# Kernel tuning notes

Hardware: AMD Instinct MI355X
Metric: run time of the kernel (lower is better)

The kernel has to match this reference:

```python
import jax, jax.numpy as jnp
import numpy as np

B, S, D = 4, 4096, 1024
BLOCK_LEN = 128
NUM_BLOCKS = S // BLOCK_LEN  # 32


def setup_inputs() -> dict:
    key = jax.random.key(0)
    k0, k1, k2 = jax.random.split(key, 3)
    x = jax.random.normal(k0, (B, S, D), dtype=jnp.float32)
    # nn.Linear weights stored as (in, out) for x @ W + b convention
    Wqkv = jax.random.normal(k1, (D, 3 * D), dtype=jnp.float32) * (1.0 / np.sqrt(D))
    bqkv = jnp.zeros((3 * D,), dtype=jnp.float32)
    Wout = jax.random.normal(k2, (D, D), dtype=jnp.float32) * (1.0 / np.sqrt(D))
    bout = jnp.zeros((D,), dtype=jnp.float32)
    return {"x": x, "Wqkv": Wqkv, "bqkv": bqkv, "Wout": Wout, "bout": bout}


def _causal_attn(q, k, v):
    # q,k,v: (..., L, D); single-head SDPA with scale 1/sqrt(D), causal mask
    d = q.shape[-1]
    L = q.shape[-2]
    scale = 1.0 / np.sqrt(d)
    scores = jnp.einsum('...qd,...kd->...qk', q, k) * jnp.asarray(scale, q.dtype)
    mask = jnp.tril(jnp.ones((L, L), dtype=bool))
    neg = jnp.asarray(jnp.finfo(scores.dtype).min, scores.dtype)
    scores = jnp.where(mask, scores, neg)
    p = jax.nn.softmax(scores, axis=-1)
    return jnp.einsum('...qk,...kd->...qd', p, v)


def reference(x, Wqkv, bqkv, Wout, bout):
    b, s, d = x.shape
    nb = s // BLOCK_LEN
    x2 = x.reshape(b, nb, BLOCK_LEN, d)              # (B, NB, BL, D)
    qkv = x2 @ Wqkv + bqkv                            # (B, NB, BL, 3D)
    q, k, v = jnp.split(qkv, 3, axis=-1)
    # 'column' attention: attend across blocks at the same within-block position
    q = q.transpose(0, 2, 1, 3)                       # (B, BL, NB, D)
    k = k.transpose(0, 2, 1, 3)
    v = v.transpose(0, 2, 1, 3)
    out = _causal_attn(q, k, v)                       # (B, BL, NB, D)
    out = out.transpose(0, 2, 1, 3).reshape(b, s, d)  # back to (B, S, D)
    return out @ Wout + bout
```

## Files before the change

kernel.cpp:

```cpp
#include <hip/hip_runtime.h>
#include <math.h>

#define BB   4
#define SS   4096
#define DD   1024
#define BL   128
#define NB   32

typedef __attribute__((ext_vector_type(4))) float f32x4;
typedef __attribute__((ext_vector_type(16))) float f32x16;
typedef __attribute__((ext_vector_type(8))) short bf16x8;
typedef __attribute__((ext_vector_type(8))) unsigned short u16x8;

__device__ __forceinline__ float bf2f(unsigned short u) {
    return __uint_as_float(((unsigned int)u) << 16);
}
__device__ __forceinline__ unsigned short f2bf(float f) {
    unsigned int u = __float_as_uint(f);
    return (unsigned short)((u + 0x7FFFu + ((u >> 16) & 1u)) >> 16);
}
__device__ __forceinline__ void gload_lds16(const unsigned short* g, unsigned short* l) {
    __builtin_amdgcn_global_load_lds(
        (const __attribute__((address_space(1))) void*)g,
        (__attribute__((address_space(3))) void*)l, 16, 0, 0);
}

__global__ __launch_bounds__(256) void cvt_f32_bf16(const float4* __restrict__ in,
                                                    ushort4* __restrict__ out, int n4) {
    int i = blockIdx.x * 256 + threadIdx.x;
    if (i < n4) {
        float4 v = in[i];
        ushort4 o;
        o.x = f2bf(v.x); o.y = f2bf(v.y); o.z = f2bf(v.z); o.w = f2bf(v.w);
        out[i] = o;
    }
}

__global__ __launch_bounds__(256) void transcvt(const float* __restrict__ W,
                                                unsigned short* __restrict__ WT,
                                                int K, int N) {
    __shared__ float tile[32][33];
    const int n0 = blockIdx.x * 32, k0 = blockIdx.y * 32;
    const int tx = threadIdx.x & 31, ty = threadIdx.x >> 5;
    #pragma unroll
    for (int r = 0; r < 32; r += 8)
        tile[ty + r][tx] = W[(size_t)(k0 + ty + r) * N + n0 + tx];
    __syncthreads();
    #pragma unroll
    for (int r = 0; r < 32; r += 8)
        WT[(size_t)(n0 + ty + r) * K + k0 + tx] = f2bf(tile[tx][ty + r]);
}

#define GBAR() __builtin_amdgcn_s_barrier()
#define LGKM0() do { asm volatile("s_waitcnt lgkmcnt(0)" ::: "memory"); \
                     __builtin_amdgcn_sched_barrier(0); } while (0)

#define MFMA_PAIR(q, ni) \
    acc[(q)*2+0][ni] = __builtin_amdgcn_mfma_f32_16x16x32_bf16(a[0][0], breg[ni][0], acc[(q)*2+0][ni], 0, 0, 0); \
    acc[(q)*2+0][ni] = __builtin_amdgcn_mfma_f32_16x16x32_bf16(a[0][1], breg[ni][1], acc[(q)*2+0][ni], 0, 0, 0); \
    acc[(q)*2+1][ni] = __builtin_amdgcn_mfma_f32_16x16x32_bf16(a[1][0], breg[ni][0], acc[(q)*2+1][ni], 0, 0, 0); \
    acc[(q)*2+1][ni] = __builtin_amdgcn_mfma_f32_16x16x32_bf16(a[1][1], breg[ni][1], acc[(q)*2+1][ni], 0, 0, 0);

#define MFMA_Q(q) do { \
    __builtin_amdgcn_s_setprio(1); \
    MFMA_PAIR(q, 0) MFMA_PAIR(q, 1) MFMA_PAIR(q, 2) MFMA_PAIR(q, 3) \
    __builtin_amdgcn_s_setprio(0); } while (0)

#define LOAD_A(q) do { \
    a[0][0] = *(const bf16x8*)(pA + ((q)*2+0)*1024 + sw0); \
    a[0][1] = *(const bf16x8*)(pA + ((q)*2+0)*1024 + sw1); \
    a[1][0] = *(const bf16x8*)(pA + ((q)*2+1)*1024 + sw0); \
    a[1][1] = *(const bf16x8*)(pA + ((q)*2+1)*1024 + sw1); } while (0)

template<typename OutT>
__global__ __launch_bounds__(512, 2) void gemm256(
    const unsigned short* __restrict__ A, const unsigned short* __restrict__ BT,
    const float* __restrict__ bias, OutT* __restrict__ C,
    int M, int N, int K, int ntn)
{
    __shared__ __align__(16) unsigned short smem[65536];
    unsigned short* sAb = smem;
    unsigned short* sBb = smem + 32768;

    const int nwg = gridDim.x;
    const int wg  = blockIdx.x;
    const int swzb = (wg & 7) * (nwg >> 3) + (wg >> 3);
    const int m0 = (swzb / ntn) * 256, n0 = (swzb % ntn) * 256;

    const int t    = threadIdx.x;
    const int w    = t >> 6;
    const int lane = t & 63;
    const int wm   = w >> 2, wn = w & 3;

    const int srow8 = lane >> 3;
    const int sgch  = (lane & 7) ^ srow8;
    const int NT    = K >> 6;

    auto STAGE_A = [&](int ts, int cb) {
        const int r = cb + (w << 3);
        gload_lds16(A + (size_t)(m0 + r + srow8) * K + (ts << 6) + sgch * 8,
                    sAb + (size_t)(ts & 1) * 16384 + r * 64);
    };
    auto STAGE_B = [&](int ts, int cb) {
        const int r = cb + (w << 3);
        gload_lds16(BT + (size_t)(n0 + r + srow8) * K + (ts << 6) + sgch * 8,
                    sBb + (size_t)(ts & 1) * 16384 + r * 64);
    };

    const int frA = wm * 128 + (lane & 15);
    const int frB = wn * 64  + (lane & 15);
    const int sw0 = (((lane >> 4) + 0) ^ (lane & 7)) * 8;
    const int sw1 = (((lane >> 4) + 4) ^ (lane & 7)) * 8;

    f32x4 acc[8][4];
    #pragma unroll
    for (int i = 0; i < 8; ++i)
        #pragma unroll
        for (int j = 0; j < 4; ++j) acc[i][j] = (f32x4){0.f, 0.f, 0.f, 0.f};

    STAGE_B(0, 0); STAGE_B(0, 64); STAGE_B(0, 128); STAGE_B(0, 192);
    STAGE_A(0, 0); STAGE_A(0, 64); STAGE_A(0, 128); STAGE_A(0, 192);
    asm volatile("s_waitcnt vmcnt(4)" ::: "memory");
    if (NT > 1) {
        STAGE_B(1, 0); STAGE_B(1, 64); STAGE_B(1, 128); STAGE_B(1, 192);
        STAGE_A(1, 0); STAGE_A(1, 128);
        asm volatile("s_waitcnt vmcnt(6)" ::: "memory");
    } else {
        asm volatile("s_waitcnt vmcnt(0)" ::: "memory");
    }
    GBAR();

    for (int ts = 0; ts < NT; ++ts) {
        const unsigned short* pA = sAb + (size_t)(ts & 1) * 16384 + frA * 64;
        const unsigned short* pB = sBb + (size_t)(ts & 1) * 16384 + frB * 64;
        bf16x8 breg[4][2];
        bf16x8 a[2][2];

        #pragma unroll
        for (int ni = 0; ni < 4; ++ni) {
            breg[ni][0] = *(const bf16x8*)(pB + ni * 1024 + sw0);
            breg[ni][1] = *(const bf16x8*)(pB + ni * 1024 + sw1);
        }
        LOAD_A(0);
        if (ts + 1 < NT) { STAGE_A(ts + 1, 64); STAGE_A(ts + 1, 192); }
        GBAR(); LGKM0(); MFMA_Q(0); GBAR();

        LOAD_A(1);
        if (ts + 2 < NT) { STAGE_B(ts + 2, 0); STAGE_B(ts + 2, 64); }
        GBAR(); LGKM0(); MFMA_Q(1); GBAR();

        LOAD_A(2);
        if (ts + 2 < NT) { STAGE_B(ts + 2, 128); STAGE_B(ts + 2, 192); }
        GBAR(); LGKM0(); MFMA_Q(2); GBAR();

        LOAD_A(3);
        if (ts + 2 < NT) { STAGE_A(ts + 2, 0); STAGE_A(ts + 2, 128); }
        GBAR(); LGKM0(); MFMA_Q(3);
        if (ts + 2 < NT) asm volatile("s_waitcnt vmcnt(6)" ::: "memory");
        else             asm volatile("s_waitcnt vmcnt(0)" ::: "memory");
        GBAR();
    }

    if constexpr (sizeof(OutT) == 2) {
        unsigned short (*cb)[256] = (unsigned short (*)[256])smem;
        #pragma unroll
        for (int ni = 0; ni < 4; ++ni) {
            const int col = wn * 64 + ni * 16 + (lane & 15);
            const float bv = bias[n0 + col];
            #pragma unroll
            for (int mi = 0; mi < 8; ++mi) {
                const int rb = wm * 128 + mi * 16 + ((lane >> 4) << 2);
                #pragma unroll
                for (int r = 0; r < 4; ++r)
                    cb[rb + r][col] = f2bf(acc[mi][ni][r] + bv);
            }
        }
        __syncthreads();
        unsigned short* Cp = (unsigned short*)C;
        #pragma unroll
        for (int it = 0; it < 16; ++it) {
            const int row = it * 16 + (t >> 5);
            const int cs  = (t & 31) * 8;
            u16x8 v = *(const u16x8*)&cb[row][cs];
            *(u16x8*)(Cp + (size_t)(m0 + row) * N + n0 + cs) = v;
        }
    } else {
        float (*cf)[256] = (float (*)[256])smem;
        #pragma unroll
        for (int h = 0; h < 2; ++h) {
            if (wm == h) {
                #pragma unroll
                for (int ni = 0; ni < 4; ++ni) {
                    const int col = wn * 64 + ni * 16 + (lane & 15);
                    const float bv = bias[n0 + col];
                    #pragma unroll
                    for (int mi = 0; mi < 8; ++mi) {
                        const int rb = mi * 16 + ((lane >> 4) << 2);
                        #pragma unroll
                        for (int r = 0; r < 4; ++r)
                            cf[rb + r][col] = acc[mi][ni][r] + bv;
                    }
                }
            }
            __syncthreads();
            float* Cp = (float*)C;
            #pragma unroll
            for (int it = 0; it < 16; ++it) {
                const int row = it * 8 + (t >> 6);
                const int c4  = (t & 63) * 4;
                float4 v = *(const float4*)&cf[row][c4];
                *(float4*)(Cp + (size_t)(m0 + h * 128 + row) * N + n0 + c4) = v;
            }
            __syncthreads();
        }
    }
}

__global__ __launch_bounds__(256) void col_attn_mfma(const unsigned short* __restrict__ qkv,
                                                     unsigned short* __restrict__ outb)
{
    const int b  = blockIdx.x >> 7;
    const int bl = blockIdx.x & (BL - 1);

    __shared__ float red[4][32][33];
    __shared__ float p_s[NB][NB + 1];

    const int t    = threadIdx.x;
    const int w    = t >> 6;
    const int lane = t & 63;

    const size_t rowstride = (size_t)BL * 3 * DD;
    const unsigned short* base = qkv + ((size_t)b * NB * BL + bl) * (3 * DD);

    {
        const int arow = lane & 31;
        const int khi  = (lane >> 5) * 8;
        const unsigned short* qp = base + (size_t)arow * rowstride + w * 256 + khi;
        const unsigned short* kp = qp + DD;

        f32x16 acc0 = {}, acc1 = {};
        #pragma unroll
        for (int s = 0; s < 16; s += 2) {
            bf16x8 aq0 = *(const bf16x8*)(qp + s * 16);
            bf16x8 bk0 = *(const bf16x8*)(kp + s * 16);
            bf16x8 aq1 = *(const bf16x8*)(qp + s * 16 + 16);
            bf16x8 bk1 = *(const bf16x8*)(kp + s * 16 + 16);
            acc0 = __builtin_amdgcn_mfma_f32_32x32x16_bf16(aq0, bk0, acc0, 0, 0, 0);
            acc1 = __builtin_amdgcn_mfma_f32_32x32x16_bf16(aq1, bk1, acc1, 0, 0, 0);
        }
        const int ccol = lane & 31;
        const int rhi  = (lane >> 5) * 4;
        #pragma unroll
        for (int r = 0; r < 16; ++r) {
            const int crow = (r & 3) + 8 * (r >> 2) + rhi;
            red[w][crow][ccol] = acc0[r] + acc1[r];
        }
    }
    __syncthreads();

    {
        const float scale = 1.0f / 32.0f;
        const int row = t >> 3;
        const int c0  = (t & 7) * 4;
        #pragma unroll
        for (int j = 0; j < 4; ++j) {
            const int c = c0 + j;
            p_s[row][c] = (red[0][row][c] + red[1][row][c] +
                           red[2][row][c] + red[3][row][c]) * scale;
        }
    }
    __syncthreads();

    if (t < NB) {
        const int i = t;
        float mx = p_s[i][0];
        for (int j = 1; j <= i; ++j) mx = fmaxf(mx, p_s[i][j]);
        float sum = 0.f;
        for (int j = 0; j <= i; ++j) { float e = __expf(p_s[i][j] - mx); p_s[i][j] = e; sum += e; }
        const float inv = 1.0f / sum;
        for (int j = 0; j <= i; ++j) p_s[i][j] *= inv;
        for (int j = i + 1; j < NB; ++j) p_s[i][j] = 0.f;
    }
    __syncthreads();

    const int d0v = t * 4;
    const unsigned short* vbase = base + 2 * DD;
    #pragma unroll 1
    for (int p = 0; p < 4; ++p) {
        float4 acc[8];
        #pragma unroll
        for (int ii = 0; ii < 8; ++ii) acc[ii] = make_float4(0.f, 0.f, 0.f, 0.f);
        const int jmax = (p + 1) * 8;
        for (int j = 0; j < jmax; ++j) {
            ushort4 v4 = *(const ushort4*)(vbase + (size_t)j * rowstride + d0v);
            const float vx = bf2f(v4.x), vy = bf2f(v4.y), vz = bf2f(v4.z), vw = bf2f(v4.w);
            #pragma unroll
            for (int ii = 0; ii < 8; ++ii) {
                const float pij = p_s[p * 8 + ii][j];
                acc[ii].x += pij * vx;
                acc[ii].y += pij * vy;
                acc[ii].z += pij * vz;
                acc[ii].w += pij * vw;
            }
        }
        #pragma unroll
        for (int ii = 0; ii < 8; ++ii) {
            const int i = p * 8 + ii;
            ushort4 o;
            o.x = f2bf(acc[ii].x); o.y = f2bf(acc[ii].y);
            o.z = f2bf(acc[ii].z); o.w = f2bf(acc[ii].w);
            *(ushort4*)(outb + ((size_t)(b * NB + i) * BL + bl) * DD + d0v) = o;
        }
    }
}

extern "C" void kernel_launch(void* const* d_in, const int* in_sizes, int n_in,
                              void* d_out, int out_size, void* d_ws, size_t ws_size,
                              hipStream_t stream) {
    (void)in_sizes; (void)n_in; (void)out_size; (void)ws_size;
    const float* x    = (const float*)d_in[0];
    const float* Wqkv = (const float*)d_in[1];
    const float* bqkv = (const float*)d_in[2];
    const float* Wout = (const float*)d_in[3];
    const float* bout = (const float*)d_in[4];
    float* out = (float*)d_out;

    char* ws = (char*)d_ws;
    unsigned short* xb    = (unsigned short*)ws;
    unsigned short* WqkvT = (unsigned short*)(ws + ((size_t)32 << 20));
    unsigned short* WoutT = (unsigned short*)(ws + ((size_t)38 << 20));
    unsigned short* qkvb  = (unsigned short*)(ws + ((size_t)40 << 20));
    unsigned short* attnb = (unsigned short*)(ws + ((size_t)136 << 20));

    const int M = BB * SS;

    cvt_f32_bf16<<<dim3((M * DD / 4 + 255) / 256), dim3(256), 0, stream>>>(
        (const float4*)x, (ushort4*)xb, M * DD / 4);
    transcvt<<<dim3(3 * DD / 32, DD / 32), dim3(256), 0, stream>>>(Wqkv, WqkvT, DD, 3 * DD);
    transcvt<<<dim3(DD / 32, DD / 32), dim3(256), 0, stream>>>(Wout, WoutT, DD, DD);

    gemm256<unsigned short><<<dim3((M / 256) * (3 * DD / 256)), dim3(512), 0, stream>>>(
        xb, WqkvT, bqkv, qkvb, M, 3 * DD, DD, 3 * DD / 256);

    col_attn_mfma<<<dim3(BB * BL), dim3(256), 0, stream>>>(qkvb, attnb);

    gemm256<float><<<dim3((M / 256) * (DD / 256)), dim3(512), 0, stream>>>(
        attnb, WoutT, bout, out, M, DD, DD, DD / 256);
}
```

Baseline: 216.5 us.

## Fuse fp32-to-bf16 conversion of x into the QKV GEMM A-tile staging

Drops the separate cvt_f32_bf16 kernel. The QKV GEMM now reads fp32 x directly through registers, converts to bf16 and writes the swizzled tile into LDS, interleaved across the four MFMA quarter-steps. This removes one kernel launch and the write and re-read of a 32MB bf16 copy of x. In exchange the A loads become register-staged rather than direct global-to-LDS, which raises register pressure and can expose load latency, since the explicit vmcnt waits are dropped for this path.

```diff
diff --git a/kernel.cpp b/kernel.cpp
--- a/kernel.cpp
+++ b/kernel.cpp
@@ -23,17 +23,6 @@
     __builtin_amdgcn_global_load_lds(
         (const __attribute__((address_space(1))) void*)g,
         (__attribute__((address_space(3))) void*)l, 16, 0, 0);
-}
-
-__global__ __launch_bounds__(256) void cvt_f32_bf16(const float4* __restrict__ in,
-                                                    ushort4* __restrict__ out, int n4) {
-    int i = blockIdx.x * 256 + threadIdx.x;
-    if (i < n4) {
-        float4 v = in[i];
-        ushort4 o;
-        o.x = f2bf(v.x); o.y = f2bf(v.y); o.z = f2bf(v.z); o.w = f2bf(v.w);
-        out[i] = o;
-    }
 }
 
 __global__ __launch_bounds__(256) void transcvt(const float* __restrict__ W,
@@ -51,6 +40,7 @@
         WT[(size_t)(n0 + ty + r) * K + k0 + tx] = f2bf(tile[tx][ty + r]);
 }
 
+
 #define GBAR() __builtin_amdgcn_s_barrier()
 #define LGKM0() do { asm volatile("s_waitcnt lgkmcnt(0)" ::: "memory"); \
                      __builtin_amdgcn_sched_barrier(0); } while (0)
@@ -72,9 +62,10 @@
     a[1][0] = *(const bf16x8*)(pA + ((q)*2+1)*1024 + sw0); \
     a[1][1] = *(const bf16x8*)(pA + ((q)*2+1)*1024 + sw1); } while (0)
 
-template<typename OutT>
+template<typename OutT, bool AF32>
 __global__ __launch_bounds__(512, 2) void gemm256(
-    const unsigned short* __restrict__ A, const unsigned short* __restrict__ BT,
+    const unsigned short* __restrict__ Abf, const float* __restrict__ Af,
+    const unsigned short* __restrict__ BT,
     const float* __restrict__ bias, OutT* __restrict__ C,
     int M, int N, int K, int ntn)
 {
@@ -98,7 +89,7 @@
 
     auto STAGE_A = [&](int ts, int cb) {
         const int r = cb + (w << 3);
-        gload_lds16(A + (size_t)(m0 + r + srow8) * K + (ts << 6) + sgch * 8,
+        gload_lds16(Abf + (size_t)(m0 + r + srow8) * K + (ts << 6) + sgch * 8,
                     sAb + (size_t)(ts & 1) * 16384 + r * 64);
     };
     auto STAGE_B = [&](int ts, int cb) {
@@ -106,6 +97,19 @@
         gload_lds16(BT + (size_t)(n0 + r + srow8) * K + (ts << 6) + sgch * 8,
                     sBb + (size_t)(ts & 1) * 16384 + r * 64);
     };
+    auto ISSUE_AQ = [&](int q, int ts1, float4& ra, float4& rb) {
+        const float* g = Af + (size_t)(m0 + q * 64 + (w << 3) + srow8) * K
+                         + (ts1 << 6) + sgch * 8;
+        ra = *(const float4*)g;
+        rb = *(const float4*)(g + 4);
+    };
+    auto WRITE_AQ = [&](int q, int ts1, const float4& ra, const float4& rb) {
+        u16x8 o;
+        o[0] = f2bf(ra.x); o[1] = f2bf(ra.y); o[2] = f2bf(ra.z); o[3] = f2bf(ra.w);
+        o[4] = f2bf(rb.x); o[5] = f2bf(rb.y); o[6] = f2bf(rb.z); o[7] = f2bf(rb.w);
+        *(u16x8*)(sAb + (size_t)(ts1 & 1) * 16384
+                  + (q * 64 + (w << 3) + srow8) * 64 + (lane & 7) * 8) = o;
+    };
 
     const int frA = wm * 128 + (lane & 15);
     const int frB = wn * 64  + (lane & 15);
@@ -118,15 +122,28 @@
         #pragma unroll
         for (int j = 0; j < 4; ++j) acc[i][j] = (f32x4){0.f, 0.f, 0.f, 0.f};
 
-    STAGE_B(0, 0); STAGE_B(0, 64); STAGE_B(0, 128); STAGE_B(0, 192);
-    STAGE_A(0, 0); STAGE_A(0, 64); STAGE_A(0, 128); STAGE_A(0, 192);
-    asm volatile("s_waitcnt vmcnt(4)" ::: "memory");
-    if (NT > 1) {
-        STAGE_B(1, 0); STAGE_B(1, 64); STAGE_B(1, 128); STAGE_B(1, 192);
-        STAGE_A(1, 0); STAGE_A(1, 128);
-        asm volatile("s_waitcnt vmcnt(6)" ::: "memory");
+    float4 r0a, r0b, r1a, r1b;
+
+    if constexpr (AF32) {
+        STAGE_B(0, 0); STAGE_B(0, 64); STAGE_B(0, 128); STAGE_B(0, 192);
+        if (NT > 1) { STAGE_B(1, 0); STAGE_B(1, 64); STAGE_B(1, 128); STAGE_B(1, 192); }
+        float4 p0a, p0b, p1a, p1b, p2a, p2b, p3a, p3b;
+        ISSUE_AQ(0, 0, p0a, p0b); ISSUE_AQ(1, 0, p1a, p1b);
+        ISSUE_AQ(2, 0, p2a, p2b); ISSUE_AQ(3, 0, p3a, p3b);
+        WRITE_AQ(0, 0, p0a, p0b); WRITE_AQ(1, 0, p1a, p1b);
+        WRITE_AQ(2, 0, p2a, p2b); WRITE_AQ(3, 0, p3a, p3b);
+        LGKM0();
     } else {
-        asm volatile("s_waitcnt vmcnt(0)" ::: "memory");
+        STAGE_B(0, 0); STAGE_B(0, 64); STAGE_B(0, 128); STAGE_B(0, 192);
+        STAGE_A(0, 0); STAGE_A(0, 64); STAGE_A(0, 128); STAGE_A(0, 192);
+        asm volatile("s_waitcnt vmcnt(4)" ::: "memory");
+        if (NT > 1) {
+            STAGE_B(1, 0); STAGE_B(1, 64); STAGE_B(1, 128); STAGE_B(1, 192);
+            STAGE_A(1, 0); STAGE_A(1, 128);
+            asm volatile("s_waitcnt vmcnt(6)" ::: "memory");
+        } else {
+            asm volatile("s_waitcnt vmcnt(0)" ::: "memory");
+        }
     }
     GBAR();
 
@@ -142,22 +159,37 @@
             breg[ni][1] = *(const bf16x8*)(pB + ni * 1024 + sw1);
         }
         LOAD_A(0);
-        if (ts + 1 < NT) { STAGE_A(ts + 1, 64); STAGE_A(ts + 1, 192); }
+        if constexpr (AF32) {
+            if (ts + 1 < NT) ISSUE_AQ(0, ts + 1, r0a, r0b);
+            if (ts > 0)      WRITE_AQ(3, ts, r1a, r1b);
+        } else {
+            if (ts + 1 < NT) { STAGE_A(ts + 1, 64); STAGE_A(ts + 1, 192); }
+        }
         GBAR(); LGKM0(); MFMA_Q(0); GBAR();
 
         LOAD_A(1);
+        if constexpr (AF32) { if (ts + 1 < NT) ISSUE_AQ(1, ts + 1, r1a, r1b); }
         if (ts + 2 < NT) { STAGE_B(ts + 2, 0); STAGE_B(ts + 2, 64); }
+        if constexpr (AF32) { if (ts + 1 < NT) WRITE_AQ(0, ts + 1, r0a, r0b); }
         GBAR(); LGKM0(); MFMA_Q(1); GBAR();
 
         LOAD_A(2);
+        if constexpr (AF32) { if (ts + 1 < NT) ISSUE_AQ(2, ts + 1, r0a, r0b); }
         if (ts + 2 < NT) { STAGE_B(ts + 2, 128); STAGE_B(ts + 2, 192); }
+        if constexpr (AF32) { if (ts + 1 < NT) WRITE_AQ(1, ts + 1, r1a, r1b); }
         GBAR(); LGKM0(); MFMA_Q(2); GBAR();
 
         LOAD_A(3);
-        if (ts + 2 < NT) { STAGE_A(ts + 2, 0); STAGE_A(ts + 2, 128); }
+        if constexpr (AF32) {
+            if (ts + 1 < NT) { ISSUE_AQ(3, ts + 1, r1a, r1b); WRITE_AQ(2, ts + 1, r0a, r0b); }
+        } else {
+            if (ts + 2 < NT) { STAGE_A(ts + 2, 0); STAGE_A(ts + 2, 128); }
+        }
         GBAR(); LGKM0(); MFMA_Q(3);
-        if (ts + 2 < NT) asm volatile("s_waitcnt vmcnt(6)" ::: "memory");
-        else             asm volatile("s_waitcnt vmcnt(0)" ::: "memory");
+        if constexpr (!AF32) {
+            if (ts + 2 < NT) asm volatile("s_waitcnt vmcnt(6)" ::: "memory");
+            else             asm volatile("s_waitcnt vmcnt(0)" ::: "memory");
+        }
         GBAR();
     }
 
@@ -326,7 +358,6 @@
     float* out = (float*)d_out;
 
     char* ws = (char*)d_ws;
-    unsigned short* xb    = (unsigned short*)ws;
     unsigned short* WqkvT = (unsigned short*)(ws + ((size_t)32 << 20));
     unsigned short* WoutT = (unsigned short*)(ws + ((size_t)38 << 20));
     unsigned short* qkvb  = (unsigned short*)(ws + ((size_t)40 << 20));
@@ -334,16 +365,14 @@
 
     const int M = BB * SS;
 
-    cvt_f32_bf16<<<dim3((M * DD / 4 + 255) / 256), dim3(256), 0, stream>>>(
-        (const float4*)x, (ushort4*)xb, M * DD / 4);
     transcvt<<<dim3(3 * DD / 32, DD / 32), dim3(256), 0, stream>>>(Wqkv, WqkvT, DD, 3 * DD);
     transcvt<<<dim3(DD / 32, DD / 32), dim3(256), 0, stream>>>(Wout, WoutT, DD, DD);
 
-    gemm256<unsigned short><<<dim3((M / 256) * (3 * DD / 256)), dim3(512), 0, stream>>>(
-        xb, WqkvT, bqkv, qkvb, M, 3 * DD, DD, 3 * DD / 256);
+    gemm256<unsigned short, true><<<dim3((M / 256) * (3 * DD / 256)), dim3(512), 0, stream>>>(
+        nullptr, x, WqkvT, bqkv, qkvb, M, 3 * DD, DD, 3 * DD / 256);
 
     col_attn_mfma<<<dim3(BB * BL), dim3(256), 0, stream>>>(qkvb, attnb);
 
-    gemm256<float><<<dim3((M / 256) * (DD / 256)), dim3(512), 0, stream>>>(
-        attnb, WoutT, bout, out, M, DD, DD, DD / 256);
-}
+    gemm256<float, false><<<dim3((M / 256) * (DD / 256)), dim3(512), 0, stream>>>(
+        attnb, nullptr, WoutT, bout, out, M, DD, DD, DD / 256);
+}
```

Result: slower. 272.1 us (+25.6%).

## Software-pipeline LDS fragment reads with double-buffered registers in GEMM main loop

Applied to the files above, without the earlier changes.

Restructures the GEMM main loop so LDS reads of the next A quarter (and the next tile's B fragments) are issued before the current quarter's MFMAs, using ping-pong A registers and two B register sets with the loop unrolled by two. Partial lgkmcnt waits replace full drains, and the extra barrier before each MFMA block is removed, so LDS latency overlaps matrix math. This costs more VGPRs, which may pressure occupancy at launch bounds (512,2). It also assumes NT is even and relies on a carefully counted vmcnt/lgkmcnt ordering.

```diff
diff --git a/kernel.cpp b/kernel.cpp
--- a/kernel.cpp
+++ b/kernel.cpp
@@ -51,26 +51,67 @@
         WT[(size_t)(n0 + ty + r) * K + k0 + tx] = f2bf(tile[tx][ty + r]);
 }
 
+
 #define GBAR() __builtin_amdgcn_s_barrier()
-#define LGKM0() do { asm volatile("s_waitcnt lgkmcnt(0)" ::: "memory"); \
+#define LGKM(n) do { asm volatile("s_waitcnt lgkmcnt(" #n ")" ::: "memory"); \
                      __builtin_amdgcn_sched_barrier(0); } while (0)
 
-#define MFMA_PAIR(q, ni) \
-    acc[(q)*2+0][ni] = __builtin_amdgcn_mfma_f32_16x16x32_bf16(a[0][0], breg[ni][0], acc[(q)*2+0][ni], 0, 0, 0); \
-    acc[(q)*2+0][ni] = __builtin_amdgcn_mfma_f32_16x16x32_bf16(a[0][1], breg[ni][1], acc[(q)*2+0][ni], 0, 0, 0); \
-    acc[(q)*2+1][ni] = __builtin_amdgcn_mfma_f32_16x16x32_bf16(a[1][0], breg[ni][0], acc[(q)*2+1][ni], 0, 0, 0); \
-    acc[(q)*2+1][ni] = __builtin_amdgcn_mfma_f32_16x16x32_bf16(a[1][1], breg[ni][1], acc[(q)*2+1][ni], 0, 0, 0);
-
-#define MFMA_Q(q) do { \
+#define MFMA_PAIR2(AR, BR, q, ni) \
+    acc[(q)*2+0][ni] = __builtin_amdgcn_mfma_f32_16x16x32_bf16(AR[0][0], BR[ni][0], acc[(q)*2+0][ni], 0, 0, 0); \
+    acc[(q)*2+0][ni] = __builtin_amdgcn_mfma_f32_16x16x32_bf16(AR[0][1], BR[ni][1], acc[(q)*2+0][ni], 0, 0, 0); \
+    acc[(q)*2+1][ni] = __builtin_amdgcn_mfma_f32_16x16x32_bf16(AR[1][0], BR[ni][0], acc[(q)*2+1][ni], 0, 0, 0); \
+    acc[(q)*2+1][ni] = __builtin_amdgcn_mfma_f32_16x16x32_bf16(AR[1][1], BR[ni][1], acc[(q)*2+1][ni], 0, 0, 0);
+
+#define MFMA_Q(AR, BR, q) do { \
     __builtin_amdgcn_s_setprio(1); \
-    MFMA_PAIR(q, 0) MFMA_PAIR(q, 1) MFMA_PAIR(q, 2) MFMA_PAIR(q, 3) \
+    MFMA_PAIR2(AR, BR, q, 0) MFMA_PAIR2(AR, BR, q, 1) \
+    MFMA_PAIR2(AR, BR, q, 2) MFMA_PAIR2(AR, BR, q, 3) \
     __builtin_amdgcn_s_setprio(0); } while (0)
 
-#define LOAD_A(q) do { \
-    a[0][0] = *(const bf16x8*)(pA + ((q)*2+0)*1024 + sw0); \
-    a[0][1] = *(const bf16x8*)(pA + ((q)*2+0)*1024 + sw1); \
-    a[1][0] = *(const bf16x8*)(pA + ((q)*2+1)*1024 + sw0); \
-    a[1][1] = *(const bf16x8*)(pA + ((q)*2+1)*1024 + sw1); } while (0)
+#define READ_AQ(dst, pA_, q) do { \
+    dst[0][0] = *(const bf16x8*)((pA_) + ((q)*2+0)*1024 + sw0); \
+    dst[0][1] = *(const bf16x8*)((pA_) + ((q)*2+0)*1024 + sw1); \
+    dst[1][0] = *(const bf16x8*)((pA_) + ((q)*2+1)*1024 + sw0); \
+    dst[1][1] = *(const bf16x8*)((pA_) + ((q)*2+1)*1024 + sw1); } while (0)
+
+#define READ_B8(dst, pB_) do { \
+    dst[0][0] = *(const bf16x8*)((pB_) + 0*1024 + sw0); \
+    dst[0][1] = *(const bf16x8*)((pB_) + 0*1024 + sw1); \
+    dst[1][0] = *(const bf16x8*)((pB_) + 1*1024 + sw0); \
+    dst[1][1] = *(const bf16x8*)((pB_) + 1*1024 + sw1); \
+    dst[2][0] = *(const bf16x8*)((pB_) + 2*1024 + sw0); \
+    dst[2][1] = *(const bf16x8*)((pB_) + 2*1024 + sw1); \
+    dst[3][0] = *(const bf16x8*)((pB_) + 3*1024 + sw0); \
+    dst[3][1] = *(const bf16x8*)((pB_) + 3*1024 + sw1); } while (0)
+
+#define TILE_BODY(ts, bC, bN) do { \
+    const unsigned short* pAc = sAb + (size_t)((ts) & 1) * 16384 + frA * 64; \
+    const unsigned short* pAn = sAb + (size_t)(((ts) + 1) & 1) * 16384 + frA * 64; \
+    const unsigned short* pBn = sBb + (size_t)(((ts) + 1) & 1) * 16384 + frB * 64; \
+     \
+    READ_AQ(aY, pAc, 1); \
+    if ((ts) + 1 < NT) { STAGE_A((ts) + 1, 64); STAGE_A((ts) + 1, 192); } \
+    LGKM(4); MFMA_Q(aX, bC, 0); GBAR(); \
+     \
+    READ_AQ(aX, pAc, 2); \
+    if ((ts) + 2 < NT) { STAGE_B((ts) + 2, 0); STAGE_B((ts) + 2, 64); } \
+    LGKM(4); MFMA_Q(aY, bC, 1); GBAR(); \
+     \
+    READ_AQ(aY, pAc, 3); \
+    if ((ts) + 2 < NT) { STAGE_B((ts) + 2, 128); STAGE_B((ts) + 2, 192); } \
+    LGKM(4); MFMA_Q(aX, bC, 2); GBAR(); \
+     \
+    if ((ts) + 1 < NT) { \
+        if ((ts) + 2 < NT) { asm volatile("s_waitcnt vmcnt(4)" ::: "memory"); } \
+        else               { asm volatile("s_waitcnt vmcnt(0)" ::: "memory"); } \
+        READ_B8(bN, pBn); READ_AQ(aX, pAn, 0); \
+        if ((ts) + 2 < NT) { STAGE_A((ts) + 2, 0); STAGE_A((ts) + 2, 128); } \
+        LGKM(12); MFMA_Q(aY, bC, 3); \
+    } else { \
+        LGKM(0); MFMA_Q(aY, bC, 3); \
+    } \
+    GBAR(); \
+} while (0)
 
 template<typename OutT>
 __global__ __launch_bounds__(512, 2) void gemm256(
@@ -118,47 +159,29 @@
         #pragma unroll
         for (int j = 0; j < 4; ++j) acc[i][j] = (f32x4){0.f, 0.f, 0.f, 0.f};
 
+    bf16x8 bgA[4][2], bgB[4][2];
+    bf16x8 aX[2][2], aY[2][2];
+
     STAGE_B(0, 0); STAGE_B(0, 64); STAGE_B(0, 128); STAGE_B(0, 192);
     STAGE_A(0, 0); STAGE_A(0, 64); STAGE_A(0, 128); STAGE_A(0, 192);
-    asm volatile("s_waitcnt vmcnt(4)" ::: "memory");
     if (NT > 1) {
         STAGE_B(1, 0); STAGE_B(1, 64); STAGE_B(1, 128); STAGE_B(1, 192);
-        STAGE_A(1, 0); STAGE_A(1, 128);
-        asm volatile("s_waitcnt vmcnt(6)" ::: "memory");
+        asm volatile("s_waitcnt vmcnt(4)" ::: "memory");
     } else {
         asm volatile("s_waitcnt vmcnt(0)" ::: "memory");
     }
     GBAR();
-
-    for (int ts = 0; ts < NT; ++ts) {
-        const unsigned short* pA = sAb + (size_t)(ts & 1) * 16384 + frA * 64;
-        const unsigned short* pB = sBb + (size_t)(ts & 1) * 16384 + frB * 64;
-        bf16x8 breg[4][2];
-        bf16x8 a[2][2];
-
-        #pragma unroll
-        for (int ni = 0; ni < 4; ++ni) {
-            breg[ni][0] = *(const bf16x8*)(pB + ni * 1024 + sw0);
-            breg[ni][1] = *(const bf16x8*)(pB + ni * 1024 + sw1);
-        }
-        LOAD_A(0);
-        if (ts + 1 < NT) { STAGE_A(ts + 1, 64); STAGE_A(ts + 1, 192); }
-        GBAR(); LGKM0(); MFMA_Q(0); GBAR();
-
-        LOAD_A(1);
-        if (ts + 2 < NT) { STAGE_B(ts + 2, 0); STAGE_B(ts + 2, 64); }
-        GBAR(); LGKM0(); MFMA_Q(1); GBAR();
-
-        LOAD_A(2);
-        if (ts + 2 < NT) { STAGE_B(ts + 2, 128); STAGE_B(ts + 2, 192); }
-        GBAR(); LGKM0(); MFMA_Q(2); GBAR();
-
-        LOAD_A(3);
-        if (ts + 2 < NT) { STAGE_A(ts + 2, 0); STAGE_A(ts + 2, 128); }
-        GBAR(); LGKM0(); MFMA_Q(3);
-        if (ts + 2 < NT) asm volatile("s_waitcnt vmcnt(6)" ::: "memory");
-        else             asm volatile("s_waitcnt vmcnt(0)" ::: "memory");
-        GBAR();
+    {
+        const unsigned short* pB0 = sBb + frB * 64;
+        const unsigned short* pA0 = sAb + frA * 64;
+        READ_B8(bgA, pB0);
+        READ_AQ(aX, pA0, 0);
+    }
+    if (NT > 1) { STAGE_A(1, 0); STAGE_A(1, 128); }
+
+    for (int ts = 0; ts < NT; ts += 2) {
+        TILE_BODY(ts, bgA, bgB);
+        TILE_BODY(ts + 1, bgB, bgA);
     }
 
     if constexpr (sizeof(OutT) == 2) {
```

New measurement: 356.4 us. +64.6%, slower.

## Double-buffer A fragments in registers and relax LDS waits in GEMM loop

Applied to the files above, without the earlier changes.

Reworks the GEMM main loop so that each quarter's A fragments are read from LDS while the previous quarter's MFMAs run, ping-ponging between two register sets. All B fragments are loaded once per K-tile. Full lgkmcnt(0) waits become partial lgkmcnt(4) waits, several workgroup barriers are removed, and the next tile's first A quarter is prefetched at the end of the current one. Launch bounds drop from two to one workgroup per CU, allowing more registers per thread at the cost of occupancy. The prefetch of the next buffer follows a per-wave vmcnt wait with no barrier, so data loaded into LDS by other waves may not be visible yet, which risks a race.

```diff
diff --git a/kernel.cpp b/kernel.cpp
--- a/kernel.cpp
+++ b/kernel.cpp
@@ -51,29 +51,41 @@
         WT[(size_t)(n0 + ty + r) * K + k0 + tx] = f2bf(tile[tx][ty + r]);
 }
 
+
 #define GBAR() __builtin_amdgcn_s_barrier()
-#define LGKM0() do { asm volatile("s_waitcnt lgkmcnt(0)" ::: "memory"); \
+#define LGKM(n) do { asm volatile("s_waitcnt lgkmcnt(" #n ")" ::: "memory"); \
                      __builtin_amdgcn_sched_barrier(0); } while (0)
 
-#define MFMA_PAIR(q, ni) \
-    acc[(q)*2+0][ni] = __builtin_amdgcn_mfma_f32_16x16x32_bf16(a[0][0], breg[ni][0], acc[(q)*2+0][ni], 0, 0, 0); \
-    acc[(q)*2+0][ni] = __builtin_amdgcn_mfma_f32_16x16x32_bf16(a[0][1], breg[ni][1], acc[(q)*2+0][ni], 0, 0, 0); \
-    acc[(q)*2+1][ni] = __builtin_amdgcn_mfma_f32_16x16x32_bf16(a[1][0], breg[ni][0], acc[(q)*2+1][ni], 0, 0, 0); \
-    acc[(q)*2+1][ni] = __builtin_amdgcn_mfma_f32_16x16x32_bf16(a[1][1], breg[ni][1], acc[(q)*2+1][ni], 0, 0, 0);
-
-#define MFMA_Q(q) do { \
+#define MFMA_PAIR2(AR, q, ni) \
+    acc[(q)*2+0][ni] = __builtin_amdgcn_mfma_f32_16x16x32_bf16(AR[0][0], bC[ni][0], acc[(q)*2+0][ni], 0, 0, 0); \
+    acc[(q)*2+0][ni] = __builtin_amdgcn_mfma_f32_16x16x32_bf16(AR[0][1], bC[ni][1], acc[(q)*2+0][ni], 0, 0, 0); \
+    acc[(q)*2+1][ni] = __builtin_amdgcn_mfma_f32_16x16x32_bf16(AR[1][0], bC[ni][0], acc[(q)*2+1][ni], 0, 0, 0); \
+    acc[(q)*2+1][ni] = __builtin_amdgcn_mfma_f32_16x16x32_bf16(AR[1][1], bC[ni][1], acc[(q)*2+1][ni], 0, 0, 0);
+
+#define MFMA_Q(AR, q) do { \
     __builtin_amdgcn_s_setprio(1); \
-    MFMA_PAIR(q, 0) MFMA_PAIR(q, 1) MFMA_PAIR(q, 2) MFMA_PAIR(q, 3) \
+    MFMA_PAIR2(AR, q, 0) MFMA_PAIR2(AR, q, 1) \
+    MFMA_PAIR2(AR, q, 2) MFMA_PAIR2(AR, q, 3) \
     __builtin_amdgcn_s_setprio(0); } while (0)
 
-#define LOAD_A(q) do { \
-    a[0][0] = *(const bf16x8*)(pA + ((q)*2+0)*1024 + sw0); \
-    a[0][1] = *(const bf16x8*)(pA + ((q)*2+0)*1024 + sw1); \
-    a[1][0] = *(const bf16x8*)(pA + ((q)*2+1)*1024 + sw0); \
-    a[1][1] = *(const bf16x8*)(pA + ((q)*2+1)*1024 + sw1); } while (0)
+#define READ_AQ(dst, pA_, q) do { \
+    dst[0][0] = *(const bf16x8*)((pA_) + ((q)*2+0)*1024 + sw0); \
+    dst[0][1] = *(const bf16x8*)((pA_) + ((q)*2+0)*1024 + sw1); \
+    dst[1][0] = *(const bf16x8*)((pA_) + ((q)*2+1)*1024 + sw0); \
+    dst[1][1] = *(const bf16x8*)((pA_) + ((q)*2+1)*1024 + sw1); } while (0)
+
+#define READ_B8(pB_) do { \
+    bC[0][0] = *(const bf16x8*)((pB_) + 0*1024 + sw0); \
+    bC[0][1] = *(const bf16x8*)((pB_) + 0*1024 + sw1); \
+    bC[1][0] = *(const bf16x8*)((pB_) + 1*1024 + sw0); \
+    bC[1][1] = *(const bf16x8*)((pB_) + 1*1024 + sw1); \
+    bC[2][0] = *(const bf16x8*)((pB_) + 2*1024 + sw0); \
+    bC[2][1] = *(const bf16x8*)((pB_) + 2*1024 + sw1); \
+    bC[3][0] = *(const bf16x8*)((pB_) + 3*1024 + sw0); \
+    bC[3][1] = *(const bf16x8*)((pB_) + 3*1024 + sw1); } while (0)
 
 template<typename OutT>
-__global__ __launch_bounds__(512, 2) void gemm256(
+__global__ __launch_bounds__(512, 1) void gemm256(
     const unsigned short* __restrict__ A, const unsigned short* __restrict__ BT,
     const float* __restrict__ bias, OutT* __restrict__ C,
     int M, int N, int K, int ntn)
@@ -118,9 +130,11 @@
         #pragma unroll
         for (int j = 0; j < 4; ++j) acc[i][j] = (f32x4){0.f, 0.f, 0.f, 0.f};
 
+    bf16x8 bC[4][2];
+    bf16x8 aX[2][2], aY[2][2];
+
     STAGE_B(0, 0); STAGE_B(0, 64); STAGE_B(0, 128); STAGE_B(0, 192);
     STAGE_A(0, 0); STAGE_A(0, 64); STAGE_A(0, 128); STAGE_A(0, 192);
-    asm volatile("s_waitcnt vmcnt(4)" ::: "memory");
     if (NT > 1) {
         STAGE_B(1, 0); STAGE_B(1, 64); STAGE_B(1, 128); STAGE_B(1, 192);
         STAGE_A(1, 0); STAGE_A(1, 128);
@@ -129,35 +143,35 @@
         asm volatile("s_waitcnt vmcnt(0)" ::: "memory");
     }
     GBAR();
+    READ_AQ(aX, sAb + frA * 64, 0);
 
     for (int ts = 0; ts < NT; ++ts) {
-        const unsigned short* pA = sAb + (size_t)(ts & 1) * 16384 + frA * 64;
-        const unsigned short* pB = sBb + (size_t)(ts & 1) * 16384 + frB * 64;
-        bf16x8 breg[4][2];
-        bf16x8 a[2][2];
-
-        #pragma unroll
-        for (int ni = 0; ni < 4; ++ni) {
-            breg[ni][0] = *(const bf16x8*)(pB + ni * 1024 + sw0);
-            breg[ni][1] = *(const bf16x8*)(pB + ni * 1024 + sw1);
-        }
-        LOAD_A(0);
+        const unsigned short* pAc = sAb + (size_t)(ts & 1) * 16384 + frA * 64;
+        const unsigned short* pAn = sAb + (size_t)((ts + 1) & 1) * 16384 + frA * 64;
+        const unsigned short* pBc = sBb + (size_t)(ts & 1) * 16384 + frB * 64;
+
+        READ_B8(pBc);
+        READ_AQ(aY, pAc, 1);
         if (ts + 1 < NT) { STAGE_A(ts + 1, 64); STAGE_A(ts + 1, 192); }
-        GBAR(); LGKM0(); MFMA_Q(0); GBAR();
-
-        LOAD_A(1);
+        LGKM(4); MFMA_Q(aX, 0); GBAR();
+
+        READ_AQ(aX, pAc, 2);
         if (ts + 2 < NT) { STAGE_B(ts + 2, 0); STAGE_B(ts + 2, 64); }
-        GBAR(); LGKM0(); MFMA_Q(1); GBAR();
-
-        LOAD_A(2);
+        LGKM(4); MFMA_Q(aY, 1); GBAR();
+
+        READ_AQ(aY, pAc, 3);
         if (ts + 2 < NT) { STAGE_B(ts + 2, 128); STAGE_B(ts + 2, 192); }
-        GBAR(); LGKM0(); MFMA_Q(2); GBAR();
-
-        LOAD_A(3);
-        if (ts + 2 < NT) { STAGE_A(ts + 2, 0); STAGE_A(ts + 2, 128); }
-        GBAR(); LGKM0(); MFMA_Q(3);
-        if (ts + 2 < NT) asm volatile("s_waitcnt vmcnt(6)" ::: "memory");
-        else             asm volatile("s_waitcnt vmcnt(0)" ::: "memory");
+        LGKM(4); MFMA_Q(aX, 2); GBAR();
+
+        if (ts + 1 < NT) {
+            if (ts + 2 < NT) { asm volatile("s_waitcnt vmcnt(4)" ::: "memory"); }
+            else             { asm volatile("s_waitcnt vmcnt(0)" ::: "memory"); }
+            READ_AQ(aX, pAn, 0);
+            if (ts + 2 < NT) { STAGE_A(ts + 2, 0); STAGE_A(ts + 2, 128); }
+            LGKM(4); MFMA_Q(aY, 3);
+        } else {
+            LGKM(0); MFMA_Q(aY, 3);
+        }
         GBAR();
     }
 
```

Result: no change. 214.7 us (-0.8%).
